# Performance work log

Hardware: AMD Instinct MI355X
Metric: run time of the kernel (lower is better)

The kernel has to match this reference:

```python
import jax, jax.numpy as jnp
import numpy as np

MAX_M = 16


def _twiddle(n, m):
    # exp(-2i*pi*n_a*m_a / (n*m)), shape (n, m), precomputed on host (static n, m)
    a = np.outer(np.arange(n), np.arange(m))
    return jnp.asarray(np.exp(-2j * np.pi * a / (n * m)).astype(np.complex64))


def _ref_dft_real(n, H):
    # reference DFT matrix as (H, n, n, 2) real view, matching ref_dft_matrix
    a = np.outer(np.arange(n), np.arange(n))
    M = np.exp(-2j * np.pi * a / n).astype(np.complex64)  # (n, n)
    M = np.broadcast_to(M, (H, n, n))
    return jnp.asarray(np.stack([M.real, M.imag], axis=-1).astype(np.float32))


def _cooley_tukey(k, n, m, mats):
    # k: (..., H, n*m) complex; mats[p]: (H, p, p) complex
    k = k.reshape(*k.shape[:-1], m, n)                      # (..., H, m, n)
    kf = jnp.einsum('hmo,...hon->...hmn', mats[m], k)       # m-length DFTs
    kf = jnp.einsum('nm,...mn->...nm', _twiddle(n, m), kf)  # twiddle + transpose -> (..., H, n, m)
    if n <= MAX_M:
        kf = jnp.einsum('hno,...hom->...hnm', mats[n], kf)  # n-length DFTs
    else:
        kf = jnp.moveaxis(kf, -1, -3)                        # '... h n m -> ... m h n'
        kf = _cooley_tukey(kf, n // MAX_M, MAX_M, mats)
        kf = jnp.moveaxis(kf, -3, -1)                        # '... m h n -> ... h n m'
    return kf.reshape(*kf.shape[:-2], n * m)


def block_fft(x, N, mats):
    # x: (..., H, L) complex, zero-pad to N, then recursive block FFT
    L = x.shape[-1]
    if L != N:
        x = jnp.pad(x, [(0, 0)] * (x.ndim - 1) + [(0, N - L)])
    return _cooley_tukey(x, N // MAX_M, MAX_M, mats)


def block_ifft(x, N, mats):
    return jnp.conj(block_fft(jnp.conj(x), N, mats)) / N


def setup_inputs() -> dict:
    key = jax.random.key(0)
    B, H, L = 16, 512, 1024
    ku, kk, kd = jax.random.split(key, 3)
    u = jax.random.normal(ku, (B, H, L), dtype=jnp.float32)
    k = jax.random.normal(kk, (H, L), dtype=jnp.float32) / L
    D = jax.random.normal(kd, (H,), dtype=jnp.float32)
    return {
        'u': u, 'k': k, 'D': D,
        'mat_2': _ref_dft_real(2, H),
        'mat_4': _ref_dft_real(4, H),
        'mat_8': _ref_dft_real(8, H),
        'mat_16': _ref_dft_real(16, H),
    }


def reference(u, k, D, mat_2, mat_4, mat_8, mat_16):
    cplx = lambda m: (m[..., 0] + 1j * m[..., 1]).astype(jnp.complex64)
    mats = {2: cplx(mat_2), 4: cplx(mat_4), 8: cplx(mat_8), 16: cplx(mat_16)}
    L = u.shape[-1]
    N = 2 * L  # causal FFT conv length
    k_f = block_fft(k.astype(jnp.complex64), N, mats)   # (H, N)
    u_f = block_fft(u.astype(jnp.complex64), N, mats)   # (B, H, N)
    y = block_ifft(u_f * k_f, N, mats)[..., :L].real    # (B, H, L)
    return (y + u * D[:, None]).astype(jnp.float32)
```

## Files before the change

kernel.cpp:

```cpp
#include <hip/hip_runtime.h>
#include <math.h>

#define NT     128
#define NB     16
#define NH     512
#define SEQ_L  1024
#define FFT_N  2048
#define RS     0.70710678118654752f
#define C16    0.92387953251128675f
#define S16    0.38268343236508977f

#define P(x) ((x) + ((x) >> 4))
#define BUF_SZ 2176

__device__ __align__(16) float2 g_kf[(size_t)NH * FFT_N];

__device__ __forceinline__ float2 cmul(float2 a, float2 b) {
    return make_float2(a.x * b.x - a.y * b.y, a.x * b.y + a.y * b.x);
}
__device__ __forceinline__ float2 cmulj(float2 a, float2 b) {
    return make_float2(a.x * b.x + a.y * b.y, a.y * b.x - a.x * b.y);
}
__device__ __forceinline__ float2 cadd(float2 a, float2 b) { return make_float2(a.x + b.x, a.y + b.y); }
__device__ __forceinline__ float2 csub(float2 a, float2 b) { return make_float2(a.x - b.x, a.y - b.y); }

template <int SIGN>
__device__ __forceinline__ void dft4(float2 x[4]) {
    float2 s0 = cadd(x[0], x[2]), s1 = csub(x[0], x[2]);
    float2 s2 = cadd(x[1], x[3]), s3 = csub(x[1], x[3]);
    x[0] = cadd(s0, s2);
    x[2] = csub(s0, s2);
    if (SIGN < 0) {
        x[1] = make_float2(s1.x + s3.y, s1.y - s3.x);
        x[3] = make_float2(s1.x - s3.y, s1.y + s3.x);
    } else {
        x[1] = make_float2(s1.x - s3.y, s1.y + s3.x);
        x[3] = make_float2(s1.x + s3.y, s1.y - s3.x);
    }
}

template <int SIGN>
__device__ __forceinline__ void dft8(float2 x[8]) {
    float2 e0 = cadd(x[0], x[4]), e1 = cadd(x[1], x[5]);
    float2 e2 = cadd(x[2], x[6]), e3 = cadd(x[3], x[7]);
    float2 o0 = csub(x[0], x[4]), o1 = csub(x[1], x[5]);
    float2 o2 = csub(x[2], x[6]), o3 = csub(x[3], x[7]);
    float2 t1, t2, t3;
    if (SIGN < 0) {
        t1 = make_float2(RS * (o1.x + o1.y), RS * (o1.y - o1.x));
        t2 = make_float2(o2.y, -o2.x);
        t3 = make_float2(-RS * (o3.x - o3.y), -RS * (o3.x + o3.y));
    } else {
        t1 = make_float2(RS * (o1.x - o1.y), RS * (o1.x + o1.y));
        t2 = make_float2(-o2.y, o2.x);
        t3 = make_float2(RS * (-o3.x - o3.y), RS * (o3.x - o3.y));
    }
    float2 s0 = cadd(e0, e2), s1 = csub(e0, e2), s2 = cadd(e1, e3), s3 = csub(e1, e3);
    x[0] = cadd(s0, s2);
    x[4] = csub(s0, s2);
    float2 u0 = cadd(o0, t2), u1 = csub(o0, t2), u2 = cadd(t1, t3), u3 = csub(t1, t3);
    x[1] = cadd(u0, u2);
    x[5] = csub(u0, u2);
    if (SIGN < 0) {
        x[2] = make_float2(s1.x + s3.y, s1.y - s3.x);
        x[6] = make_float2(s1.x - s3.y, s1.y + s3.x);
        x[3] = make_float2(u1.x + u3.y, u1.y - u3.x);
        x[7] = make_float2(u1.x - u3.y, u1.y + u3.x);
    } else {
        x[2] = make_float2(s1.x - s3.y, s1.y + s3.x);
        x[6] = make_float2(s1.x + s3.y, s1.y - s3.x);
        x[3] = make_float2(u1.x - u3.y, u1.y + u3.x);
        x[7] = make_float2(u1.x + u3.y, u1.y - u3.x);
    }
}

template <int SIGN>
__device__ __forceinline__ void dft16_twiddle(float2 v[4][4]) {
    const float sg = (SIGN < 0) ? -1.f : 1.f;
    const float2 W1 = make_float2(C16, sg * S16);
    const float2 W2 = make_float2(RS, sg * RS);
    const float2 W3 = make_float2(S16, sg * C16);
    const float2 W6 = make_float2(-RS, sg * RS);
    const float2 W9 = make_float2(-C16, -sg * S16);
    v[1][1] = cmul(v[1][1], W1);
    v[1][2] = cmul(v[1][2], W2);
    v[1][3] = cmul(v[1][3], W3);
    v[2][1] = cmul(v[2][1], W2);
    v[2][2] = make_float2(-sg * v[2][2].y, sg * v[2][2].x);
    v[2][3] = cmul(v[2][3], W6);
    v[3][1] = cmul(v[3][1], W3);
    v[3][2] = cmul(v[3][2], W6);
    v[3][3] = cmul(v[3][3], W9);
}

template <int SIGN>
__device__ __forceinline__ void dft16(float2 x[16]) {
    float2 v[4][4];
#pragma unroll
    for (int n0 = 0; n0 < 4; ++n0) {
        float2 a[4] = {x[n0], x[n0 + 4], x[n0 + 8], x[n0 + 12]};
        dft4<SIGN>(a);
        v[n0][0] = a[0]; v[n0][1] = a[1]; v[n0][2] = a[2]; v[n0][3] = a[3];
    }
    dft16_twiddle<SIGN>(v);
#pragma unroll
    for (int k0 = 0; k0 < 4; ++k0) {
        float2 a[4] = {v[0][k0], v[1][k0], v[2][k0], v[3][k0]};
        dft4<SIGN>(a);
        x[k0] = a[0]; x[k0 + 4] = a[1]; x[k0 + 8] = a[2]; x[k0 + 12] = a[3];
    }
}

__device__ __forceinline__ void dft16_zero8(const float2 z[8], float2 x[16]) {
    float2 v[4][4];
#pragma unroll
    for (int n0 = 0; n0 < 4; ++n0) {
        float2 a = z[n0], b = z[n0 + 4];
        v[n0][0] = cadd(a, b);
        v[n0][1] = make_float2(a.x + b.y, a.y - b.x);
        v[n0][2] = csub(a, b);
        v[n0][3] = make_float2(a.x - b.y, a.y + b.x);
    }
    dft16_twiddle<-1>(v);
#pragma unroll
    for (int k0 = 0; k0 < 4; ++k0) {
        float2 a[4] = {v[0][k0], v[1][k0], v[2][k0], v[3][k0]};
        dft4<-1>(a);
        x[k0] = a[0]; x[k0 + 4] = a[1]; x[k0 + 8] = a[2]; x[k0 + 12] = a[3];
    }
}

__device__ __forceinline__ void dft16_inv_low8(const float2 x[16], float2 y[8]) {
    float2 v[4][4];
#pragma unroll
    for (int n0 = 0; n0 < 4; ++n0) {
        float2 a[4] = {x[n0], x[n0 + 4], x[n0 + 8], x[n0 + 12]};
        dft4<+1>(a);
        v[n0][0] = a[0]; v[n0][1] = a[1]; v[n0][2] = a[2]; v[n0][3] = a[3];
    }
    dft16_twiddle<+1>(v);
#pragma unroll
    for (int k0 = 0; k0 < 4; ++k0) {
        float2 x0 = v[0][k0], x1 = v[1][k0], x2 = v[2][k0], x3 = v[3][k0];
        float2 s0 = cadd(x0, x2), s1 = csub(x0, x2);
        float2 s2 = cadd(x1, x3), s3 = csub(x1, x3);
        y[k0]     = cadd(s0, s2);
        y[k0 + 4] = make_float2(s1.x - s3.y, s1.y + s3.x);
    }
}

__global__ __launch_bounds__(NT, 2) void kfft_kernel(const float* __restrict__ kin) {
    __shared__ float re[BUF_SZ];
    __shared__ float im[BUF_SZ];
    __shared__ float2 twlds[NT];
    const int t = threadIdx.x;
    const int h = blockIdx.x;
    float2 w1;
    {
        float sv, cv;
        sincosf(-6.283185307179586f * (float)t / (float)FFT_N, &sv, &cv);
        w1 = make_float2(cv, sv);
        twlds[t] = w1;
    }
    const float* krow = kin + (size_t)h * SEQ_L;
    {
        float2 z[8], x[16];
#pragma unroll
        for (int j = 0; j < 8; ++j) z[j] = make_float2(krow[t + 128 * j], 0.f);
        dft16_zero8(z, x);
        float2 w = w1;
#pragma unroll
        for (int c = 1; c < 16; ++c) { x[c] = cmul(x[c], w); w = cmul(w, w1); }
#pragma unroll
        for (int c = 0; c < 16; ++c) {
            const int id = P(t + 128 * c);
            re[id] = x[c].x; im[id] = x[c].y;
        }
    }
    __syncthreads();
    const int cblk = t >> 3, r = t & 7;
    const int base = 128 * cblk + r;
    {
        float2 x[16];
#pragma unroll
        for (int j = 0; j < 16; ++j) {
            const int id = P(base + 8 * j);
            x[j] = make_float2(re[id], im[id]);
        }
        dft16<-1>(x);
        const float2 ws = twlds[16 * r];
        float2 w = ws;
#pragma unroll
        for (int c2 = 1; c2 < 16; ++c2) { x[c2] = cmul(x[c2], w); w = cmul(w, ws); }
#pragma unroll
        for (int c2 = 0; c2 < 16; ++c2) {
            const int id = P(base + 8 * c2);
            re[id] = x[c2].x; im[id] = x[c2].y;
        }
    }
    __syncthreads();
#pragma unroll
    for (int gi = 0; gi < 2; ++gi) {
        const int g = 2 * t + gi;
        float2 x[8];
#pragma unroll
        for (int l = 0; l < 8; ++l) {
            const int id = P(8 * g + l);
            x[l] = make_float2(re[id], im[id]);
        }
        dft8<-1>(x);
        float4* o4 = (float4*)(g_kf + (size_t)h * FFT_N + 8 * g);
#pragma unroll
        for (int l = 0; l < 4; ++l)
            o4[l] = make_float4(x[2 * l].x, x[2 * l].y, x[2 * l + 1].x, x[2 * l + 1].y);
    }
}

__global__ __launch_bounds__(NT, 2) void conv_pair_kernel(const float* __restrict__ u,
                                                          const float* __restrict__ D,
                                                          float* __restrict__ out) {
    __shared__ float re[BUF_SZ];
    __shared__ float im[BUF_SZ];
    __shared__ float2 twlds[NT];
    const int t = threadIdx.x;
    const int h = blockIdx.x & (NH - 1);
    const int bp = blockIdx.x >> 9;
    const size_t row0 = (size_t)(2 * bp) * NH + h;
    const size_t row1 = row0 + NH;
    float2 w1;
    {
        float sv, cv;
        sincosf(-6.283185307179586f * (float)t / (float)FFT_N, &sv, &cv);
        w1 = make_float2(cv, sv);
        twlds[t] = w1;
    }
    const float* u0 = u + row0 * SEQ_L;
    const float* u1 = u + row1 * SEQ_L;
    {
        float2 z[8], x[16];
#pragma unroll
        for (int j = 0; j < 8; ++j)
            z[j] = make_float2(u0[t + 128 * j], u1[t + 128 * j]);
        dft16_zero8(z, x);
        float2 w = w1;
#pragma unroll
        for (int c = 1; c < 16; ++c) { x[c] = cmul(x[c], w); w = cmul(w, w1); }
#pragma unroll
        for (int c = 0; c < 16; ++c) {
            const int id = P(t + 128 * c);
            re[id] = x[c].x; im[id] = x[c].y;
        }
    }
    __syncthreads();
    const int cblk = t >> 3, r = t & 7;
    const int base = 128 * cblk + r;
    const float2 ws = twlds[16 * r];
    {
        float2 x[16];
#pragma unroll
        for (int j = 0; j < 16; ++j) {
            const int id = P(base + 8 * j);
            x[j] = make_float2(re[id], im[id]);
        }
        dft16<-1>(x);
        float2 w = ws;
#pragma unroll
        for (int c2 = 1; c2 < 16; ++c2) { x[c2] = cmul(x[c2], w); w = cmul(w, ws); }
#pragma unroll
        for (int c2 = 0; c2 < 16; ++c2) {
            const int id = P(base + 8 * c2);
            re[id] = x[c2].x; im[id] = x[c2].y;
        }
    }
    __syncthreads();
    {
        const float2* kfr = g_kf + (size_t)h * FFT_N;
#pragma unroll
        for (int gi = 0; gi < 2; ++gi) {
            const int g = 2 * t + gi;
            float2 x[8];
#pragma unroll
            for (int l = 0; l < 8; ++l) {
                const int id = P(8 * g + l);
                x[l] = make_float2(re[id], im[id]);
            }
            dft8<-1>(x);
            const float4* k4 = (const float4*)(kfr + 8 * g);
#pragma unroll
            for (int l = 0; l < 4; ++l) {
                float4 kk = k4[l];
                x[2 * l]     = cmul(x[2 * l],     make_float2(kk.x, kk.y));
                x[2 * l + 1] = cmul(x[2 * l + 1], make_float2(kk.z, kk.w));
            }
            dft8<+1>(x);
#pragma unroll
            for (int l = 0; l < 8; ++l) {
                const int id = P(8 * g + l);
                re[id] = x[l].x; im[id] = x[l].y;
            }
        }
    }
    __syncthreads();
    {
        float2 x[16];
#pragma unroll
        for (int c2 = 0; c2 < 16; ++c2) {
            const int id = P(base + 8 * c2);
            x[c2] = make_float2(re[id], im[id]);
        }
        float2 w = ws;
#pragma unroll
        for (int c2 = 1; c2 < 16; ++c2) { x[c2] = cmulj(x[c2], w); w = cmul(w, ws); }
        dft16<+1>(x);
#pragma unroll
        for (int j = 0; j < 16; ++j) {
            const int id = P(base + 8 * j);
            re[id] = x[j].x; im[id] = x[j].y;
        }
    }
    __syncthreads();
    {
        float2 x[16];
#pragma unroll
        for (int c = 0; c < 16; ++c) {
            const int id = P(t + 128 * c);
            x[c] = make_float2(re[id], im[id]);
        }
        float2 w = w1;
#pragma unroll
        for (int c = 1; c < 16; ++c) { x[c] = cmulj(x[c], w); w = cmul(w, w1); }
        float2 y[8];
        dft16_inv_low8(x, y);
        const float Dh = D[h];
        const float invN = 1.0f / (float)FFT_N;
        float* o0row = out + row0 * SEQ_L;
        float* o1row = out + row1 * SEQ_L;
#pragma unroll
        for (int j = 0; j < 8; ++j) {
            o0row[t + 128 * j] = y[j].x * invN + u0[t + 128 * j] * Dh;
            o1row[t + 128 * j] = y[j].y * invN + u1[t + 128 * j] * Dh;
        }
    }
}

extern "C" void kernel_launch(void* const* d_in, const int* in_sizes, int n_in,
                              void* d_out, int out_size, void* d_ws, size_t ws_size,
                              hipStream_t stream) {
    const float* u = (const float*)d_in[0];
    const float* k = (const float*)d_in[1];
    const float* D = (const float*)d_in[2];
    float* out = (float*)d_out;

    kfft_kernel<<<NH, NT, 0, stream>>>(k);
    conv_pair_kernel<<<NB * NH / 2, NT, 0, stream>>>(u, D, out);
}
```

Baseline: 113.4 us.

## Fuse kernel FFT into conv kernel, keep spectrum in registers across batch pairs

Merges the separate k-FFT kernel and the convolution kernel into one launch. Each block recomputes the filter spectrum for its channel, keeps it in registers, and loops over several batch pairs. This removes the global round-trip of the filter spectrum and one kernel launch. Twiddle powers now use a shallower multiplication tree, and launch bounds rise to 3 blocks per CU. In exchange, the k-FFT is computed redundantly three times per channel, and the grid shrinks to 1536 blocks with uneven per-block work (3/3/2 batch pairs). The extra registers held for the spectrum may also limit occupancy.

```diff
diff --git a/kernel.cpp b/kernel.cpp
--- a/kernel.cpp
+++ b/kernel.cpp
@@ -12,8 +12,6 @@
 
 #define P(x) ((x) + ((x) >> 4))
 #define BUF_SZ 2176
-
-__device__ __align__(16) float2 g_kf[(size_t)NH * FFT_N];
 
 __device__ __forceinline__ float2 cmul(float2 a, float2 b) {
     return make_float2(a.x * b.x - a.y * b.y, a.x * b.y + a.y * b.x);
@@ -149,12 +147,37 @@
     }
 }
 
-__global__ __launch_bounds__(NT, 2) void kfft_kernel(const float* __restrict__ kin) {
+template <int CONJ>
+__device__ __forceinline__ void tw_apply16(float2 x[16], float2 a) {
+#define AP(v, w) (v) = CONJ ? cmulj((v), (w)) : cmul((v), (w))
+    AP(x[1], a);
+    float2 w2 = cmul(a, a);      AP(x[2], w2);
+    float2 w3 = cmul(w2, a);     AP(x[3], w3);
+    float2 w4 = cmul(w2, w2);    AP(x[4], w4);
+    float2 w5 = cmul(w4, a);     AP(x[5], w5);
+    float2 w6 = cmul(w4, w2);    AP(x[6], w6);
+    float2 w7 = cmul(w6, a);     AP(x[7], w7);
+    float2 w8 = cmul(w4, w4);    AP(x[8], w8);
+    float2 w9 = cmul(w8, a);     AP(x[9], w9);
+    float2 w10 = cmul(w8, w2);   AP(x[10], w10);
+    float2 w11 = cmul(w10, a);   AP(x[11], w11);
+    float2 w12 = cmul(w8, w4);   AP(x[12], w12);
+    float2 w13 = cmul(w12, a);   AP(x[13], w13);
+    float2 w14 = cmul(w12, w2);  AP(x[14], w14);
+    float2 w15 = cmul(w14, a);   AP(x[15], w15);
+#undef AP
+}
+
+__global__ __launch_bounds__(NT, 3) void mono_kernel(const float* __restrict__ u,
+                                                     const float* __restrict__ kin,
+                                                     const float* __restrict__ D,
+                                                     float* __restrict__ out) {
     __shared__ float re[BUF_SZ];
     __shared__ float im[BUF_SZ];
     __shared__ float2 twlds[NT];
     const int t = threadIdx.x;
-    const int h = blockIdx.x;
+    const int h = blockIdx.x & (NH - 1);
+    const int j3 = blockIdx.x >> 9;
     float2 w1;
     {
         float sv, cv;
@@ -162,183 +185,148 @@
         w1 = make_float2(cv, sv);
         twlds[t] = w1;
     }
-    const float* krow = kin + (size_t)h * SEQ_L;
+    const int cblk = t >> 3, r = t & 7;
+    const int base = 128 * cblk + r;
+
+    float2 kreg[2][8];
     {
+        const float* krow = kin + (size_t)h * SEQ_L;
         float2 z[8], x[16];
 #pragma unroll
-        for (int j = 0; j < 8; ++j) z[j] = make_float2(krow[t + 128 * j], 0.f);
+        for (int m = 0; m < 8; ++m) z[m] = make_float2(krow[t + 128 * m], 0.f);
         dft16_zero8(z, x);
-        float2 w = w1;
-#pragma unroll
-        for (int c = 1; c < 16; ++c) { x[c] = cmul(x[c], w); w = cmul(w, w1); }
+        tw_apply16<0>(x, w1);
 #pragma unroll
         for (int c = 0; c < 16; ++c) {
             const int id = P(t + 128 * c);
             re[id] = x[c].x; im[id] = x[c].y;
         }
-    }
-    __syncthreads();
-    const int cblk = t >> 3, r = t & 7;
-    const int base = 128 * cblk + r;
-    {
-        float2 x[16];
-#pragma unroll
-        for (int j = 0; j < 16; ++j) {
-            const int id = P(base + 8 * j);
-            x[j] = make_float2(re[id], im[id]);
+        __syncthreads();
+        const float2 wsk = twlds[16 * r];
+#pragma unroll
+        for (int c = 0; c < 16; ++c) {
+            const int id = P(base + 8 * c);
+            x[c] = make_float2(re[id], im[id]);
         }
         dft16<-1>(x);
-        const float2 ws = twlds[16 * r];
-        float2 w = ws;
-#pragma unroll
-        for (int c2 = 1; c2 < 16; ++c2) { x[c2] = cmul(x[c2], w); w = cmul(w, ws); }
-#pragma unroll
-        for (int c2 = 0; c2 < 16; ++c2) {
-            const int id = P(base + 8 * c2);
-            re[id] = x[c2].x; im[id] = x[c2].y;
-        }
-    }
-    __syncthreads();
-#pragma unroll
-    for (int gi = 0; gi < 2; ++gi) {
-        const int g = 2 * t + gi;
-        float2 x[8];
-#pragma unroll
-        for (int l = 0; l < 8; ++l) {
-            const int id = P(8 * g + l);
-            x[l] = make_float2(re[id], im[id]);
-        }
-        dft8<-1>(x);
-        float4* o4 = (float4*)(g_kf + (size_t)h * FFT_N + 8 * g);
-#pragma unroll
-        for (int l = 0; l < 4; ++l)
-            o4[l] = make_float4(x[2 * l].x, x[2 * l].y, x[2 * l + 1].x, x[2 * l + 1].y);
-    }
-}
-
-__global__ __launch_bounds__(NT, 2) void conv_pair_kernel(const float* __restrict__ u,
-                                                          const float* __restrict__ D,
-                                                          float* __restrict__ out) {
-    __shared__ float re[BUF_SZ];
-    __shared__ float im[BUF_SZ];
-    __shared__ float2 twlds[NT];
-    const int t = threadIdx.x;
-    const int h = blockIdx.x & (NH - 1);
-    const int bp = blockIdx.x >> 9;
-    const size_t row0 = (size_t)(2 * bp) * NH + h;
-    const size_t row1 = row0 + NH;
-    float2 w1;
-    {
-        float sv, cv;
-        sincosf(-6.283185307179586f * (float)t / (float)FFT_N, &sv, &cv);
-        w1 = make_float2(cv, sv);
-        twlds[t] = w1;
-    }
-    const float* u0 = u + row0 * SEQ_L;
-    const float* u1 = u + row1 * SEQ_L;
-    {
-        float2 z[8], x[16];
-#pragma unroll
-        for (int j = 0; j < 8; ++j)
-            z[j] = make_float2(u0[t + 128 * j], u1[t + 128 * j]);
-        dft16_zero8(z, x);
-        float2 w = w1;
-#pragma unroll
-        for (int c = 1; c < 16; ++c) { x[c] = cmul(x[c], w); w = cmul(w, w1); }
+        tw_apply16<0>(x, wsk);
 #pragma unroll
         for (int c = 0; c < 16; ++c) {
-            const int id = P(t + 128 * c);
+            const int id = P(base + 8 * c);
             re[id] = x[c].x; im[id] = x[c].y;
         }
-    }
-    __syncthreads();
-    const int cblk = t >> 3, r = t & 7;
-    const int base = 128 * cblk + r;
-    const float2 ws = twlds[16 * r];
-    {
-        float2 x[16];
-#pragma unroll
-        for (int j = 0; j < 16; ++j) {
-            const int id = P(base + 8 * j);
-            x[j] = make_float2(re[id], im[id]);
-        }
-        dft16<-1>(x);
-        float2 w = ws;
-#pragma unroll
-        for (int c2 = 1; c2 < 16; ++c2) { x[c2] = cmul(x[c2], w); w = cmul(w, ws); }
-#pragma unroll
-        for (int c2 = 0; c2 < 16; ++c2) {
-            const int id = P(base + 8 * c2);
-            re[id] = x[c2].x; im[id] = x[c2].y;
-        }
-    }
-    __syncthreads();
-    {
-        const float2* kfr = g_kf + (size_t)h * FFT_N;
+        __syncthreads();
 #pragma unroll
         for (int gi = 0; gi < 2; ++gi) {
             const int g = 2 * t + gi;
-            float2 x[8];
+            float2 xk[8];
 #pragma unroll
             for (int l = 0; l < 8; ++l) {
                 const int id = P(8 * g + l);
-                x[l] = make_float2(re[id], im[id]);
-            }
-            dft8<-1>(x);
-            const float4* k4 = (const float4*)(kfr + 8 * g);
-#pragma unroll
-            for (int l = 0; l < 4; ++l) {
-                float4 kk = k4[l];
-                x[2 * l]     = cmul(x[2 * l],     make_float2(kk.x, kk.y));
-                x[2 * l + 1] = cmul(x[2 * l + 1], make_float2(kk.z, kk.w));
-            }
-            dft8<+1>(x);
-#pragma unroll
-            for (int l = 0; l < 8; ++l) {
-                const int id = P(8 * g + l);
-                re[id] = x[l].x; im[id] = x[l].y;
-            }
-        }
-    }
-    __syncthreads();
-    {
-        float2 x[16];
-#pragma unroll
-        for (int c2 = 0; c2 < 16; ++c2) {
-            const int id = P(base + 8 * c2);
-            x[c2] = make_float2(re[id], im[id]);
-        }
-        float2 w = ws;
-#pragma unroll
-        for (int c2 = 1; c2 < 16; ++c2) { x[c2] = cmulj(x[c2], w); w = cmul(w, ws); }
-        dft16<+1>(x);
-#pragma unroll
-        for (int j = 0; j < 16; ++j) {
-            const int id = P(base + 8 * j);
-            re[id] = x[j].x; im[id] = x[j].y;
-        }
-    }
-    __syncthreads();
-    {
-        float2 x[16];
-#pragma unroll
-        for (int c = 0; c < 16; ++c) {
-            const int id = P(t + 128 * c);
-            x[c] = make_float2(re[id], im[id]);
-        }
-        float2 w = w1;
-#pragma unroll
-        for (int c = 1; c < 16; ++c) { x[c] = cmulj(x[c], w); w = cmul(w, w1); }
-        float2 y[8];
-        dft16_inv_low8(x, y);
-        const float Dh = D[h];
-        const float invN = 1.0f / (float)FFT_N;
-        float* o0row = out + row0 * SEQ_L;
-        float* o1row = out + row1 * SEQ_L;
-#pragma unroll
-        for (int j = 0; j < 8; ++j) {
-            o0row[t + 128 * j] = y[j].x * invN + u0[t + 128 * j] * Dh;
-            o1row[t + 128 * j] = y[j].y * invN + u1[t + 128 * j] * Dh;
+                xk[l] = make_float2(re[id], im[id]);
+            }
+            dft8<-1>(xk);
+#pragma unroll
+            for (int l = 0; l < 8; ++l) kreg[gi][l] = xk[l];
+        }
+        __syncthreads();
+    }
+
+    const float2 ws = twlds[16 * r];
+    const float Dh = D[h];
+    const float invN = 1.0f / (float)FFT_N;
+
+    for (int bp = j3; bp < 8; bp += 3) {
+        if (bp != j3) __syncthreads();
+        const size_t row0 = (size_t)(2 * bp) * NH + h;
+        const size_t row1 = row0 + NH;
+        const float* u0 = u + row0 * SEQ_L;
+        const float* u1 = u + row1 * SEQ_L;
+        {
+            float2 z[8], x[16];
+#pragma unroll
+            for (int m = 0; m < 8; ++m)
+                z[m] = make_float2(u0[t + 128 * m], u1[t + 128 * m]);
+            dft16_zero8(z, x);
+            tw_apply16<0>(x, w1);
+#pragma unroll
+            for (int c = 0; c < 16; ++c) {
+                const int id = P(t + 128 * c);
+                re[id] = x[c].x; im[id] = x[c].y;
+            }
+        }
+        __syncthreads();
+        {
+            float2 x[16];
+#pragma unroll
+            for (int c = 0; c < 16; ++c) {
+                const int id = P(base + 8 * c);
+                x[c] = make_float2(re[id], im[id]);
+            }
+            dft16<-1>(x);
+            tw_apply16<0>(x, ws);
+#pragma unroll
+            for (int c = 0; c < 16; ++c) {
+                const int id = P(base + 8 * c);
+                re[id] = x[c].x; im[id] = x[c].y;
+            }
+        }
+        __syncthreads();
+        {
+#pragma unroll
+            for (int gi = 0; gi < 2; ++gi) {
+                const int g = 2 * t + gi;
+                float2 x[8];
+#pragma unroll
+                for (int l = 0; l < 8; ++l) {
+                    const int id = P(8 * g + l);
+                    x[l] = make_float2(re[id], im[id]);
+                }
+                dft8<-1>(x);
+#pragma unroll
+                for (int l = 0; l < 8; ++l) x[l] = cmul(x[l], kreg[gi][l]);
+                dft8<+1>(x);
+#pragma unroll
+                for (int l = 0; l < 8; ++l) {
+                    const int id = P(8 * g + l);
+                    re[id] = x[l].x; im[id] = x[l].y;
+                }
+            }
+        }
+        __syncthreads();
+        {
+            float2 x[16];
+#pragma unroll
+            for (int c = 0; c < 16; ++c) {
+                const int id = P(base + 8 * c);
+                x[c] = make_float2(re[id], im[id]);
+            }
+            tw_apply16<1>(x, ws);
+            dft16<+1>(x);
+#pragma unroll
+            for (int c = 0; c < 16; ++c) {
+                const int id = P(base + 8 * c);
+                re[id] = x[c].x; im[id] = x[c].y;
+            }
+        }
+        __syncthreads();
+        {
+            float2 x[16];
+#pragma unroll
+            for (int c = 0; c < 16; ++c) {
+                const int id = P(t + 128 * c);
+                x[c] = make_float2(re[id], im[id]);
+            }
+            tw_apply16<1>(x, w1);
+            float2 y[8];
+            dft16_inv_low8(x, y);
+            float* o0row = out + row0 * SEQ_L;
+            float* o1row = out + row1 * SEQ_L;
+#pragma unroll
+            for (int m = 0; m < 8; ++m) {
+                o0row[t + 128 * m] = y[m].x * invN + u0[t + 128 * m] * Dh;
+                o1row[t + 128 * m] = y[m].y * invN + u1[t + 128 * m] * Dh;
+            }
         }
     }
 }
@@ -351,6 +339,5 @@
     const float* D = (const float*)d_in[2];
     float* out = (float*)d_out;
 
-    kfft_kernel<<<NH, NT, 0, stream>>>(k);
-    conv_pair_kernel<<<NB * NH / 2, NT, 0, stream>>>(u, D, out);
-}
+    mono_kernel<<<3 * NH, NT, 0, stream>>>(u, k, D, out);
+}
```

New measurement: 154.0 us. 1.36x slower.
